# Optimization experiments

Measured on AMD Instinct MI355X. Metric: run time of the kernel, lower is better.

The kernel has to match this reference:

```python
import jax, jax.numpy as jnp
import numpy as np

N_SUPPORT = 8192
N_QUERY = 8192
INPUT_DIM = 1024
EMBED_DIM = 512
N_CLASSES = 64


def setup_inputs() -> dict:
    key = jax.random.key(0)
    k1, k2, k3, k4 = jax.random.split(key, 4)
    support_data = jax.random.normal(k1, (N_SUPPORT, INPUT_DIM), dtype=jnp.float32)
    query_data = jax.random.normal(k2, (N_QUERY, INPUT_DIM), dtype=jnp.float32)
    support_labels = jax.random.randint(k3, (N_SUPPORT,), 0, N_CLASSES, dtype=jnp.int32)
    W = jax.random.normal(k4, (INPUT_DIM, EMBED_DIM), dtype=jnp.float32) * (1.0 / np.sqrt(INPUT_DIM))
    return {"support_data": support_data, "support_labels": support_labels,
            "query_data": query_data, "W": W}


def _l2_normalize(x, eps=1e-12):
    # Matches F.normalize(p=2): x / max(||x||, eps)
    n = jnp.linalg.norm(x, axis=-1, keepdims=True)
    return x / jnp.maximum(n, eps)


def reference(support_data, support_labels, query_data, W):
    # encoder: single linear projection
    s_emb = support_data @ W            # [Ns, D]
    q_emb = query_data @ W              # [Nq, D]
    s_norm = _l2_normalize(s_emb)
    q_norm = _l2_normalize(q_emb)
    # cosine similarities for all query/support pairs: [Nq, Ns]
    sims = q_norm @ s_norm.T
    # per-class sum over support samples (torch.unique -> sorted 0..N_CLASSES-1)
    # segment_sum along the support axis: [N_classes, Nq] -> [Nq, N_classes]
    class_scores = jax.ops.segment_sum(sims.T, support_labels, num_segments=N_CLASSES).T
    return jax.nn.softmax(class_scores, axis=-1)
```

## Files before the change

kernel.cpp:

```cpp
#include <hip/hip_runtime.h>
#include <hip/hip_bf16.h>

#define NS 8192
#define NQ 8192
#define NTOT 16384
#define KDIM 1024
#define ED 512
#define NC 64
#define PBLK 64

typedef __attribute__((ext_vector_type(4))) float fx4;
typedef __attribute__((ext_vector_type(4))) int ix4;
typedef __attribute__((ext_vector_type(8))) short sx8;
typedef __attribute__((ext_vector_type(4))) unsigned short ux4;
typedef __attribute__((ext_vector_type(8))) unsigned short ux8;

__device__ __forceinline__ unsigned short f2bf(float f) {
  union { float f; unsigned u; } v; v.f = f;
  unsigned r = v.u + 0x7fffu + ((v.u >> 16) & 1u);
  return (unsigned short)(r >> 16);
}
__device__ __forceinline__ float bf2f(unsigned short h) {
  union { unsigned u; float f; } v; v.u = ((unsigned)h) << 16;
  return v.f;
}

__device__ __forceinline__ void async_ld16(const void* g, void* l) {
  __builtin_amdgcn_global_load_lds(
      (const __attribute__((address_space(1))) unsigned int*)g,
      (__attribute__((address_space(3))) unsigned int*)l, 16, 0, 0);
}

__global__ __launch_bounds__(256) void k_prep(
    const float* __restrict__ W, unsigned short* __restrict__ Wt,
    float* __restrict__ rowssq) {
  __shared__ float tile[32][33];
  int bid = blockIdx.x;
  int t = threadIdx.x;
  int k0 = (bid & 31) * 32;
  int n0 = (bid >> 5) * 32;
  int tx = t & 31, ty = t >> 5;
#pragma unroll
  for (int i = ty; i < 32; i += 8)
    tile[i][tx] = W[(size_t)(k0 + i) * ED + n0 + tx];
  __syncthreads();
#pragma unroll
  for (int i = ty; i < 32; i += 8)
    Wt[(size_t)(n0 + i) * KDIM + k0 + tx] = f2bf(tile[tx][i]);
  if (t < 32) rowssq[bid * 32 + t] = 0.f;
}

__global__ __launch_bounds__(256) void k_gemm_embed(
    const float* __restrict__ Xs, const float* __restrict__ Xq,
    const unsigned short* __restrict__ Wt,
    unsigned short* __restrict__ emb, float* __restrict__ rowssq) {
  __shared__ unsigned short Ash[2][128 * 8 * 8];
  __shared__ unsigned short Bsh[2][128 * 8 * 8];

  int lid = blockIdx.x;
  int x = lid & 7;
  int s = lid >> 3;
  int m_blk = x * 16 + (s >> 2);
  int n_blk = s & 3;

  const float* Xsrc = (m_blk < 64)
      ? (Xs + (size_t)m_blk * 128 * KDIM)
      : (Xq + (size_t)(m_blk - 64) * 128 * KDIM);
  const unsigned short* Wrow = Wt + (size_t)n_blk * 128 * KDIM;

  int t = threadIdx.x;
  int lane = t & 63, w = t >> 6;
  int wm = w >> 1, wn = w & 1;
  int quad = lane >> 4, ml = lane & 15;

  fx4 acc[4][4];
#pragma unroll
  for (int i = 0; i < 4; ++i)
#pragma unroll
    for (int j = 0; j < 4; ++j) acc[i][j] = fx4{0.f, 0.f, 0.f, 0.f};

  fx4 avA[4][2], avB[4][2];

  auto loadA = [&](int kt, fx4 (&av)[4][2]) {
    int k0 = kt * 64;
#pragma unroll
    for (int c = 0; c < 4; ++c) {
      int ch = t + 256 * c;
      int m = ch >> 3, kq = ch & 7;
      const float* g = &Xsrc[(size_t)m * KDIM + k0 + kq * 8];
      av[c][0] = *(const fx4*)g;
      av[c][1] = *(const fx4*)(g + 4);
    }
  };
  auto writeA = [&](const fx4 (&av)[4][2], int bbuf) {
#pragma unroll
    for (int c = 0; c < 4; ++c) {
      int ch = t + 256 * c;
      int m = ch >> 3, kq = ch & 7;
      ux8 o;
      o[0] = f2bf(av[c][0].x); o[1] = f2bf(av[c][0].y);
      o[2] = f2bf(av[c][0].z); o[3] = f2bf(av[c][0].w);
      o[4] = f2bf(av[c][1].x); o[5] = f2bf(av[c][1].y);
      o[6] = f2bf(av[c][1].z); o[7] = f2bf(av[c][1].w);
      *(ux8*)&Ash[bbuf][((m * 8) + (kq ^ (m & 7))) * 8] = o;
    }
  };
  auto stageB = [&](int kt, int b) {
    int k0 = kt * 64;
#pragma unroll
    for (int c = 0; c < 4; ++c) {
      int ch = t + 256 * c;
      int n = ch >> 3;
      int kq = (ch & 7) ^ (n & 7);
      async_ld16(&Wrow[(size_t)n * KDIM + k0 + kq * 8],
                 &Bsh[b][(w * 64 + 256 * c) * 8]);
    }
  };
  auto compute = [&](int b) {
#pragma unroll
    for (int s2 = 0; s2 < 2; ++s2) {
      int kq = s2 * 4 + quad;
      sx8 af[4], bfr[4];
#pragma unroll
      for (int i = 0; i < 4; ++i) {
        int row = wm * 64 + i * 16 + ml;
        af[i] = *(const sx8*)&Ash[b][(row * 8 + (kq ^ (row & 7))) * 8];
      }
#pragma unroll
      for (int j = 0; j < 4; ++j) {
        int nrow = wn * 64 + j * 16 + ml;
        bfr[j] = *(const sx8*)&Bsh[b][(nrow * 8 + (kq ^ (nrow & 7))) * 8];
      }
#pragma unroll
      for (int i = 0; i < 4; ++i)
#pragma unroll
        for (int j = 0; j < 4; ++j)
          acc[i][j] = __builtin_amdgcn_mfma_f32_16x16x32_bf16(af[i], bfr[j], acc[i][j], 0, 0, 0);
    }
  };

  stageB(0, 0);
  __builtin_amdgcn_sched_barrier(0);
  loadA(0, avA);
  loadA(1, avB);
  __builtin_amdgcn_sched_barrier(0);
  writeA(avA, 0);
  asm volatile("s_waitcnt vmcnt(8) lgkmcnt(0)" ::: "memory");
  __builtin_amdgcn_sched_barrier(0);
  __builtin_amdgcn_s_barrier();

  for (int it = 0; it < 8; ++it) {
    int kt0 = it * 2;
    stageB(kt0 + 1, 1);
    __builtin_amdgcn_sched_barrier(0);
    loadA(kt0 + 2 < 16 ? kt0 + 2 : 15, avA);

    __builtin_amdgcn_s_setprio(1);
    compute(0);
    __builtin_amdgcn_s_setprio(0);

    writeA(avB, 1);
    asm volatile("s_waitcnt vmcnt(8) lgkmcnt(0)" ::: "memory");
    __builtin_amdgcn_sched_barrier(0);
    __builtin_amdgcn_s_barrier();

    stageB(kt0 + 2 < 16 ? kt0 + 2 : 15, 0);
    __builtin_amdgcn_sched_barrier(0);
    loadA(kt0 + 3 < 16 ? kt0 + 3 : 15, avB);

    __builtin_amdgcn_s_setprio(1);
    compute(1);
    __builtin_amdgcn_s_setprio(0);

    writeA(avA, 0);
    asm volatile("s_waitcnt vmcnt(8) lgkmcnt(0)" ::: "memory");
    __builtin_amdgcn_sched_barrier(0);
    __builtin_amdgcn_s_barrier();
  }

  int grow = m_blk * 128 + wm * 64;
  int gcol = n_blk * 128 + wn * 64;
#pragma unroll
  for (int i = 0; i < 4; ++i) {
#pragma unroll
    for (int r = 0; r < 4; ++r) {
      int mrow = grow + i * 16 + quad * 4 + r;
      float p = 0.f;
#pragma unroll
      for (int j = 0; j < 4; ++j) {
        emb[(size_t)mrow * ED + gcol + j * 16 + ml] = f2bf(acc[i][j][r]);
        p += acc[i][j][r] * acc[i][j][r];
      }
#pragma unroll
      for (int off = 1; off < 16; off <<= 1) p += __shfl_xor(p, off, 16);
      if (ml == 0) atomicAdd(&rowssq[mrow], p);
    }
  }
}

__global__ __launch_bounds__(256) void k_proto_partial(
    const unsigned short* __restrict__ embS, const float* __restrict__ rowssq,
    const int* __restrict__ labels, float* __restrict__ Ppart) {
  __shared__ float Pl[NC * 64];
  int t = threadIdx.x;
#pragma unroll
  for (int i = 0; i < 16; ++i) Pl[i * 256 + t] = 0.f;
  __syncthreads();

  int w = t >> 6, lane = t & 63;
  int ds = blockIdx.y;
  int row0 = blockIdx.x * (NS / PBLK);
#pragma unroll 4
  for (int r = w; r < NS / PBLK; r += 4) {
    int row = row0 + r;
    int lbl = labels[row];
    float scale = 1.0f / fmaxf(sqrtf(rowssq[row]), 1e-12f);
    float v = bf2f(embS[(size_t)row * ED + ds * 64 + lane]) * scale;
    atomicAdd(&Pl[lbl * 64 + lane], v);
  }
  __syncthreads();

  float* o = Ppart + (size_t)blockIdx.x * NC * ED + ds * 64;
#pragma unroll
  for (int i = 0; i < 16; ++i) {
    int idx = i * 256 + t;
    o[(size_t)(idx >> 6) * ED + (idx & 63)] = Pl[idx];
  }
}

__global__ __launch_bounds__(256) void k_proto_reduce(
    const float* __restrict__ Ppart, unsigned short* __restrict__ Pbf) {
  int idx = blockIdx.x * 256 + threadIdx.x;
  int kq = idx >> 9;
  int n = (idx >> 3) & 63;
  int j = idx & 7;
  int d = kq * 8 + j;
  float s = 0.f;
#pragma unroll 8
  for (int b = 0; b < PBLK; ++b) s += Ppart[(size_t)b * NC * ED + n * ED + d];
  Pbf[idx] = f2bf(s);
}

__global__ __launch_bounds__(64) void k_scores(
    const unsigned short* __restrict__ embQ, const float* __restrict__ ssqQ,
    const unsigned short* __restrict__ Pbf, float* __restrict__ out) {
  int lane = threadIdx.x;
  int quad = lane >> 4, ml = lane & 15;
  int qrow0 = blockIdx.x * 16;

  fx4 acc[4];
#pragma unroll
  for (int i = 0; i < 4; ++i) acc[i] = fx4{0.f, 0.f, 0.f, 0.f};

#pragma unroll 4
  for (int ki = 0; ki < 16; ++ki) {
    sx8 a = *(const sx8*)&embQ[(size_t)(qrow0 + ml) * ED + ki * 32 + quad * 8];
#pragma unroll
    for (int nt = 0; nt < 4; ++nt) {
      sx8 b = *(const sx8*)&Pbf[((ki * 4 + quad) * 64 + nt * 16 + ml) * 8];
      acc[nt] = __builtin_amdgcn_mfma_f32_16x16x32_bf16(a, b, acc[nt], 0, 0, 0);
    }
  }

#pragma unroll
  for (int r = 0; r < 4; ++r) {
    int qq = qrow0 + quad * 4 + r;
    float scale = 1.0f / fmaxf(sqrtf(ssqQ[qq]), 1e-12f);
    float s[4];
#pragma unroll
    for (int nt = 0; nt < 4; ++nt) s[nt] = acc[nt][r] * scale;
    float m = fmaxf(fmaxf(s[0], s[1]), fmaxf(s[2], s[3]));
#pragma unroll
    for (int off = 1; off < 16; off <<= 1) m = fmaxf(m, __shfl_xor(m, off, 16));
    float e[4], ssum = 0.f;
#pragma unroll
    for (int nt = 0; nt < 4; ++nt) { e[nt] = __expf(s[nt] - m); ssum += e[nt]; }
#pragma unroll
    for (int off = 1; off < 16; off <<= 1) ssum += __shfl_xor(ssum, off, 16);
    float inv = 1.0f / ssum;
#pragma unroll
    for (int nt = 0; nt < 4; ++nt)
      out[(size_t)qq * NC + nt * 16 + ml] = e[nt] * inv;
  }
}

extern "C" void kernel_launch(void* const* d_in, const int* in_sizes, int n_in,
                              void* d_out, int out_size, void* d_ws, size_t ws_size,
                              hipStream_t stream) {
  const float* Xs     = (const float*)d_in[0];
  const int*   labels = (const int*)d_in[1];
  const float* Xq     = (const float*)d_in[2];
  const float* W      = (const float*)d_in[3];
  float* out = (float*)d_out;

  char* ws = (char*)d_ws;
  size_t off = 0;
  unsigned short* Wt  = (unsigned short*)(ws + off); off += (size_t)ED * KDIM * 2;
  unsigned short* emb = (unsigned short*)(ws + off); off += (size_t)NTOT * ED * 2;
  float* rowssq = (float*)(ws + off); off += (size_t)NTOT * 4;
  float* Ppart  = (float*)(ws + off); off += (size_t)PBLK * NC * ED * 4;
  unsigned short* Pbf = (unsigned short*)(ws + off); off += (size_t)NC * ED * 2;

  k_prep<<<512, 256, 0, stream>>>(W, Wt, rowssq);
  k_gemm_embed<<<512, 256, 0, stream>>>(Xs, Xq, Wt, emb, rowssq);
  k_proto_partial<<<dim3(PBLK, 8), 256, 0, stream>>>(emb, rowssq, labels, Ppart);
  k_proto_reduce<<<NC * ED / 256, 256, 0, stream>>>(Ppart, Pbf);
  k_scores<<<NQ / 16, 64, 0, stream>>>(emb + (size_t)NS * ED, rowssq + NS, Pbf, out);
}
```

Baseline: 177.3 us.

## Pre-pack W into MFMA fragment order and load B directly to registers

The prep kernel now writes W in bf16 already arranged in the per-lane MFMA B-fragment order, so the embedding GEMM loads B operands straight from global memory into registers with coalesced 16-byte loads. This removes the B shared-memory buffers, the async global-to-LDS copies and the matching LDS reads. The pipeline waits change to wait only on LDS operations, and the setprio hints are dropped. In exchange each wave fetches its B data from global or L2 without reuse through LDS, so any latency not hidden by the compute adds directly to the loop.

```diff
diff --git a/kernel.cpp b/kernel.cpp
--- a/kernel.cpp
+++ b/kernel.cpp
@@ -10,9 +10,7 @@
 #define PBLK 64
 
 typedef __attribute__((ext_vector_type(4))) float fx4;
-typedef __attribute__((ext_vector_type(4))) int ix4;
 typedef __attribute__((ext_vector_type(8))) short sx8;
-typedef __attribute__((ext_vector_type(4))) unsigned short ux4;
 typedef __attribute__((ext_vector_type(8))) unsigned short ux8;
 
 __device__ __forceinline__ unsigned short f2bf(float f) {
@@ -25,37 +23,30 @@
   return v.f;
 }
 
-__device__ __forceinline__ void async_ld16(const void* g, void* l) {
-  __builtin_amdgcn_global_load_lds(
-      (const __attribute__((address_space(1))) unsigned int*)g,
-      (__attribute__((address_space(3))) unsigned int*)l, 16, 0, 0);
-}
-
 __global__ __launch_bounds__(256) void k_prep(
-    const float* __restrict__ W, unsigned short* __restrict__ Wt,
+    const float* __restrict__ W, unsigned short* __restrict__ Wtp,
     float* __restrict__ rowssq) {
-  __shared__ float tile[32][33];
-  int bid = blockIdx.x;
-  int t = threadIdx.x;
-  int k0 = (bid & 31) * 32;
-  int n0 = (bid >> 5) * 32;
-  int tx = t & 31, ty = t >> 5;
-#pragma unroll
-  for (int i = ty; i < 32; i += 8)
-    tile[i][tx] = W[(size_t)(k0 + i) * ED + n0 + tx];
-  __syncthreads();
-#pragma unroll
-  for (int i = ty; i < 32; i += 8)
-    Wt[(size_t)(n0 + i) * KDIM + k0 + tx] = f2bf(tile[tx][i]);
-  if (t < 32) rowssq[bid * 32 + t] = 0.f;
+  int c = blockIdx.x * 256 + threadIdx.x;
+  int lane = c & 63;
+  int j    = (c >> 6) & 3;
+  int s2   = (c >> 8) & 1;
+  int kt   = (c >> 9) & 15;
+  int n64  = c >> 13;
+  int quad = lane >> 4, ml = lane & 15;
+  int n  = n64 * 64 + j * 16 + ml;
+  int kb = kt * 64 + (s2 * 4 + quad) * 8;
+  ux8 o;
+#pragma unroll
+  for (int e = 0; e < 8; ++e) o[e] = f2bf(W[(size_t)(kb + e) * ED + n]);
+  *(ux8*)&Wtp[(size_t)c * 8] = o;
+  if (c < NTOT) rowssq[c] = 0.f;
 }
 
 __global__ __launch_bounds__(256) void k_gemm_embed(
     const float* __restrict__ Xs, const float* __restrict__ Xq,
-    const unsigned short* __restrict__ Wt,
+    const unsigned short* __restrict__ Wtp,
     unsigned short* __restrict__ emb, float* __restrict__ rowssq) {
   __shared__ unsigned short Ash[2][128 * 8 * 8];
-  __shared__ unsigned short Bsh[2][128 * 8 * 8];
 
   int lid = blockIdx.x;
   int x = lid & 7;
@@ -66,12 +57,14 @@
   const float* Xsrc = (m_blk < 64)
       ? (Xs + (size_t)m_blk * 128 * KDIM)
       : (Xq + (size_t)(m_blk - 64) * 128 * KDIM);
-  const unsigned short* Wrow = Wt + (size_t)n_blk * 128 * KDIM;
 
   int t = threadIdx.x;
   int lane = t & 63, w = t >> 6;
   int wm = w >> 1, wn = w & 1;
   int quad = lane >> 4, ml = lane & 15;
+  int n64 = n_blk * 2 + wn;
+
+  const unsigned short* Bbase = Wtp + ((size_t)n64 * 8192 + lane) * 8;
 
   fx4 acc[4][4];
 #pragma unroll
@@ -105,77 +98,56 @@
       *(ux8*)&Ash[bbuf][((m * 8) + (kq ^ (m & 7))) * 8] = o;
     }
   };
-  auto stageB = [&](int kt, int b) {
-    int k0 = kt * 64;
-#pragma unroll
-    for (int c = 0; c < 4; ++c) {
-      int ch = t + 256 * c;
-      int n = ch >> 3;
-      int kq = (ch & 7) ^ (n & 7);
-      async_ld16(&Wrow[(size_t)n * KDIM + k0 + kq * 8],
-                 &Bsh[b][(w * 64 + 256 * c) * 8]);
-    }
-  };
-  auto compute = [&](int b) {
+  auto loadB = [&](int kt, sx8 (&bf)[2][4]) {
+#pragma unroll
+    for (int s2 = 0; s2 < 2; ++s2)
+#pragma unroll
+      for (int j = 0; j < 4; ++j)
+        bf[s2][j] = *(const sx8*)&Bbase[(size_t)(kt * 512 + s2 * 256 + j * 64) * 8];
+  };
+  auto compute = [&](int b, const sx8 (&bf)[2][4]) {
 #pragma unroll
     for (int s2 = 0; s2 < 2; ++s2) {
       int kq = s2 * 4 + quad;
-      sx8 af[4], bfr[4];
+      sx8 af[4];
 #pragma unroll
       for (int i = 0; i < 4; ++i) {
         int row = wm * 64 + i * 16 + ml;
         af[i] = *(const sx8*)&Ash[b][(row * 8 + (kq ^ (row & 7))) * 8];
       }
 #pragma unroll
-      for (int j = 0; j < 4; ++j) {
-        int nrow = wn * 64 + j * 16 + ml;
-        bfr[j] = *(const sx8*)&Bsh[b][(nrow * 8 + (kq ^ (nrow & 7))) * 8];
-      }
-#pragma unroll
       for (int i = 0; i < 4; ++i)
 #pragma unroll
         for (int j = 0; j < 4; ++j)
-          acc[i][j] = __builtin_amdgcn_mfma_f32_16x16x32_bf16(af[i], bfr[j], acc[i][j], 0, 0, 0);
-    }
-  };
-
-  stageB(0, 0);
-  __builtin_amdgcn_sched_barrier(0);
+          acc[i][j] = __builtin_amdgcn_mfma_f32_16x16x32_bf16(af[i], bf[s2][j], acc[i][j], 0, 0, 0);
+    }
+  };
+  auto sync_step = [&]() {
+    __builtin_amdgcn_sched_barrier(0);
+    asm volatile("s_waitcnt lgkmcnt(0)" ::: "memory");
+    __builtin_amdgcn_s_barrier();
+    __builtin_amdgcn_sched_barrier(0);
+  };
+
   loadA(0, avA);
   loadA(1, avB);
-  __builtin_amdgcn_sched_barrier(0);
   writeA(avA, 0);
-  asm volatile("s_waitcnt vmcnt(8) lgkmcnt(0)" ::: "memory");
-  __builtin_amdgcn_sched_barrier(0);
-  __builtin_amdgcn_s_barrier();
+  sync_step();
 
   for (int it = 0; it < 8; ++it) {
     int kt0 = it * 2;
-    stageB(kt0 + 1, 1);
-    __builtin_amdgcn_sched_barrier(0);
+    sx8 bf[2][4];
+    loadB(kt0, bf);
     loadA(kt0 + 2 < 16 ? kt0 + 2 : 15, avA);
-
-    __builtin_amdgcn_s_setprio(1);
-    compute(0);
-    __builtin_amdgcn_s_setprio(0);
-
+    compute(0, bf);
     writeA(avB, 1);
-    asm volatile("s_waitcnt vmcnt(8) lgkmcnt(0)" ::: "memory");
-    __builtin_amdgcn_sched_barrier(0);
-    __builtin_amdgcn_s_barrier();
-
-    stageB(kt0 + 2 < 16 ? kt0 + 2 : 15, 0);
-    __builtin_amdgcn_sched_barrier(0);
+    sync_step();
+
+    loadB(kt0 + 1, bf);
     loadA(kt0 + 3 < 16 ? kt0 + 3 : 15, avB);
-
-    __builtin_amdgcn_s_setprio(1);
-    compute(1);
-    __builtin_amdgcn_s_setprio(0);
-
+    compute(1, bf);
     writeA(avA, 0);
-    asm volatile("s_waitcnt vmcnt(8) lgkmcnt(0)" ::: "memory");
-    __builtin_amdgcn_sched_barrier(0);
-    __builtin_amdgcn_s_barrier();
+    sync_step();
   }
 
   int grow = m_blk * 128 + wm * 64;
@@ -295,14 +267,14 @@
 
   char* ws = (char*)d_ws;
   size_t off = 0;
-  unsigned short* Wt  = (unsigned short*)(ws + off); off += (size_t)ED * KDIM * 2;
+  unsigned short* Wtp = (unsigned short*)(ws + off); off += (size_t)ED * KDIM * 2;
   unsigned short* emb = (unsigned short*)(ws + off); off += (size_t)NTOT * ED * 2;
   float* rowssq = (float*)(ws + off); off += (size_t)NTOT * 4;
   float* Ppart  = (float*)(ws + off); off += (size_t)PBLK * NC * ED * 4;
   unsigned short* Pbf = (unsigned short*)(ws + off); off += (size_t)NC * ED * 2;
 
-  k_prep<<<512, 256, 0, stream>>>(W, Wt, rowssq);
-  k_gemm_embed<<<512, 256, 0, stream>>>(Xs, Xq, Wt, emb, rowssq);
+  k_prep<<<256, 256, 0, stream>>>(W, Wtp, rowssq);
+  k_gemm_embed<<<512, 256, 0, stream>>>(Xs, Xq, Wtp, emb, rowssq);
   k_proto_partial<<<dim3(PBLK, 8), 256, 0, stream>>>(emb, rowssq, labels, Ppart);
   k_proto_reduce<<<NC * ED / 256, 256, 0, stream>>>(Ppart, Pbf);
   k_scores<<<NQ / 16, 64, 0, stream>>>(emb + (size_t)NS * ED, rowssq + NS, Pbf, out);
```

Measured after the change: 172.7 us. 1.03x faster.
